# Kernel tuning notes

Measured on AMD Instinct MI355X. Metric: run time of the kernel, lower is better.

The kernel has to match this reference:

```python
import jax, jax.numpy as jnp
import numpy as np
import math

B, N, P, S, C, NC = 8, 20000, 256, 32, 256, 18


def setup_inputs() -> dict:
    key = jax.random.key(0)
    ks = jax.random.split(key, 20)
    w = lambda k, shape: jax.random.normal(k, shape, jnp.float32) * 0.02
    return {
        "xyz": jax.random.normal(ks[0], (B, N, 3), jnp.float32),
        "features": jax.random.normal(ks[1], (B, C, N), jnp.float32),
        "boxes_size": jax.random.uniform(ks[2], (B, P, 3), jnp.float32, 0.2, 1.5),
        "boxes_label": jax.random.normal(ks[3], (B, P, NC), jnp.float32),
        "ts": jax.random.uniform(ks[4], (B,), jnp.float32) * 1000.0,
        "inds": jax.random.randint(ks[5], (B, P), 0, N, jnp.int32),
        # SharedMLP (259 -> 128 -> 128 -> 128), bn=False so conv1x1+bias+ReLU
        "mw0": w(ks[6], (128, C + 3)), "mb0": jnp.zeros((128,), jnp.float32),
        "mw1": w(ks[7], (128, 128)), "mb1": jnp.zeros((128,), jnp.float32),
        "mw2": w(ks[8], (128, 128)), "mb2": jnp.zeros((128,), jnp.float32),
        # label SharedMLP (18+128 -> 256 -> 256 -> 256)
        "lw0": w(ks[9], (256, NC + 128)), "lb0": jnp.zeros((256,), jnp.float32),
        "lw1": w(ks[10], (256, 256)), "lb1": jnp.zeros((256,), jnp.float32),
        "lw2": w(ks[11], (256, 256)), "lb2": jnp.zeros((256,), jnp.float32),
        # time_mlp: sinusoid(128) -> 512 -> GELU -> 512 ; block: SiLU -> 256
        "tw0": w(ks[12], (512, 128)), "tb0": jnp.zeros((512,), jnp.float32),
        "tw1": w(ks[13], (512, 512)), "tb1": jnp.zeros((512,), jnp.float32),
        "bw": w(ks[14], (256, 512)), "bb": jnp.zeros((256,), jnp.float32),
        # time_mlp_label: sinusoid(256) -> 1024 -> GELU -> 1024 ; block: SiLU -> 512
        "tlw0": w(ks[15], (1024, 256)), "tlb0": jnp.zeros((1024,), jnp.float32),
        "tlw1": w(ks[16], (1024, 1024)), "tlb1": jnp.zeros((1024,), jnp.float32),
        "blw": w(ks[17], (512, 1024)), "blb": jnp.zeros((512,), jnp.float32),
    }


def _sinusoid(t, dim):
    half = dim // 2
    freqs = jnp.exp(jnp.arange(half, dtype=jnp.float32) * (-(math.log(10000.0) / (half - 1))))
    e = t[:, None] * freqs[None, :]
    return jnp.concatenate([jnp.sin(e), jnp.cos(e)], axis=-1)


def _film(feat, ts, w0, b0, w1, b1, bw, bb, dim):
    # feat: [B, D, P]; replicates torch repeat_interleave/chunk/reshape exactly
    temb = jax.nn.gelu(_sinusoid(ts, dim) @ w0.T + b0, approximate=False) @ w1.T + b1
    ss = jax.nn.silu(temb) @ bw.T + bb          # [B, 2D]
    ss = jnp.repeat(ss, P, axis=0)              # [B*P, 2D]
    scale, shift = jnp.split(ss, 2, axis=1)
    scale = scale.reshape(-1, P)
    shift = shift.reshape(-1, P)
    f = feat.reshape(-1, P)
    return (f * (scale + 1.0) + shift).reshape(feat.shape[0], -1, P)


def reference(xyz, features, boxes_size, boxes_label, ts, inds,
              mw0, mb0, mw1, mb1, mw2, mb2,
              lw0, lb0, lw1, lb1, lw2, lb2,
              tw0, tb0, tw1, tb1, bw, bb,
              tlw0, tlb0, tlw1, tlb1, blw, blb):
    # gather proposal centers
    new_xyz = jnp.take_along_axis(xyz, inds[:, :, None], axis=1)        # [B,P,3]
    # axis-aligned box containment (the hull corners are an AABB: center +/- size/2)
    half = boxes_size * 0.5
    inside = jnp.all(jnp.abs(xyz[:, None, :, :] - new_xyz[:, :, None, :]) <= half[:, :, None, :], axis=-1)  # [B,P,N]
    # deterministic with-replacement sampling of in-box points: in-box indices first (stable sort), then cycle
    order = jnp.argsort(jnp.logical_not(inside), axis=-1)               # [B,P,N]
    count = jnp.maximum(inside.sum(axis=-1), 1)                          # [B,P]
    pos = jnp.arange(S, dtype=count.dtype)[None, None, :] % count[:, :, None]
    idx = jnp.take_along_axis(order, pos, axis=-1)                       # [B,P,S]
    b_idx = jnp.arange(B)[:, None, None]
    gxyz = xyz[b_idx, idx] - new_xyz[:, :, None, :]                      # [B,P,S,3]
    gfeat = jnp.transpose(features, (0, 2, 1))[b_idx, idx]               # [B,P,S,C]
    g = jnp.concatenate([gxyz, gfeat], axis=-1)                          # [B,P,S,3+C]
    act = lambda x, w, b: jax.nn.relu(jnp.einsum('bpsc,oc->bpso', x, w) + b)
    h = act(act(act(g, mw0, mb0), mw1, mb1), mw2, mb2)                   # [B,P,S,128]
    nf = h.max(axis=2)                                                   # [B,P,128] (max-pool over nsample)
    nf_t = jnp.transpose(nf, (0, 2, 1))                                  # [B,128,P]
    new_features = _film(nf_t, ts, tw0, tb0, tw1, tb1, bw, bb, 128)
    # label branch
    li = jnp.concatenate([boxes_label, nf], axis=-1)                     # [B,P,18+128]
    act2 = lambda x, w, b: jax.nn.relu(jnp.einsum('bpc,oc->bpo', x, w) + b)
    lf = act2(act2(act2(li, lw0, lb0), lw1, lb1), lw2, lb2)              # [B,P,256]
    lf_t = jnp.transpose(lf, (0, 2, 1))                                  # [B,256,P]
    label_feature = _film(lf_t, ts, tlw0, tlb0, tlw1, tlb1, blw, blb, 256)
    return (new_xyz, new_features, label_feature, inds)
```

## Files before the change

kernel.cpp:

```cpp
#include <hip/hip_runtime.h>
#include <math.h>

#define BB 8
#define NN 20000
#define PP 256
#define SSAMP 32
#define CC 256

typedef unsigned short u16;
typedef unsigned int u32;
typedef __attribute__((ext_vector_type(8))) short short8;
typedef __attribute__((ext_vector_type(4))) float f32x4;

struct __align__(4) f3v { float x, y, z; };

__device__ __forceinline__ float b2f(u16 u) {
    union { u32 i; float f; } x; x.i = ((u32)u) << 16; return x.f;
}
__device__ __forceinline__ u16 f2b(float f) {
    union { float f; u32 i; } x; x.f = f;
    u32 i = x.i;
    i += 0x7fffu + ((i >> 16) & 1u);
    return (u16)(i >> 16);
}
__device__ __forceinline__ float rnd_bf(float f) { return b2f(f2b(f)); }
__device__ __forceinline__ float geluf(float x) {
    return 0.5f * x * (1.0f + erff(x * 0.7071067811865476f));
}
__device__ __forceinline__ float siluf(float x) {
    return x / (1.0f + expf(-x));
}
__device__ __forceinline__ f32x4 fz4() { f32x4 z = {0.f,0.f,0.f,0.f}; return z; }

__device__ __forceinline__ float ldf(const void* p, size_t i, int f32f) {
    return f32f ? ((const float*)p)[i] : b2f(((const u16*)p)[i]);
}
__device__ __forceinline__ u16 ldw(const void* p, size_t i, int f32f) {
    return f32f ? f2b(((const float*)p)[i]) : ((const u16*)p)[i];
}

__device__ __forceinline__ int detect_f32d(const void* xyz) {
    int lane = threadIdx.x & 63;
    u16 u = ((const u16*)xyz)[(size_t)lane * 7496];
    int e = (u >> 7) & 0xFF;
    bool inR = (e >= 0x70) && (e <= 0x85);
    unsigned long long m = __ballot(inR);
    return (__popcll(m) < 48) ? 1 : 0;
}

__device__ __forceinline__ void repack_body(int f32f, int rb, int tid,
        const void* mw0, const void* mw1, const void* mw2,
        const void* lw0, const void* lw1, const void* lw2,
        const void* mb0, const void* mb1, const void* mb2,
        const void* lb0, const void* lb1, const void* lb2,
        u16* __restrict__ W0p, u16* __restrict__ W1p, u16* __restrict__ W2p,
        u16* __restrict__ L0p, u16* __restrict__ L1p, u16* __restrict__ L2p,
        float* __restrict__ biasF) {
    int i = rb * 256 + tid;
    if (i < 36864) {
        int o = i / 288, c = i % 288;
        u16 v = 0;
        if (c < 256) v = ldw(mw0, o * 259 + 3 + c, f32f);
        else if (c < 259) v = ldw(mw0, o * 259 + (c - 256), f32f);
        W0p[i] = v;
    } else if (i < 53248) {
        W1p[i - 36864] = ldw(mw1, i - 36864, f32f);
    } else if (i < 69632) {
        W2p[i - 53248] = ldw(mw2, i - 53248, f32f);
    } else if (i < 110592) {
        int j = i - 69632;
        int o = j / 160, c = j % 160;
        L0p[j] = (c < 146) ? ldw(lw0, o * 146 + c, f32f) : (u16)0;
    } else if (i < 176128) {
        L1p[i - 110592] = ldw(lw1, i - 110592, f32f);
    } else if (i < 241664) {
        L2p[i - 176128] = ldw(lw2, i - 176128, f32f);
    } else if (i < 242816) {
        int j = i - 241664;
        float v;
        if (j < 128) v = ldf(mb0, j, f32f);
        else if (j < 256) v = ldf(mb1, j - 128, f32f);
        else if (j < 384) v = ldf(mb2, j - 256, f32f);
        else if (j < 640) v = ldf(lb0, j - 384, f32f);
        else if (j < 896) v = ldf(lb1, j - 640, f32f);
        else v = ldf(lb2, j - 896, f32f);
        biasF[j] = v;
    }
}

__device__ __forceinline__ void transpose_body(int f32f, const void* __restrict__ feat,
        u16* __restrict__ featT, int n0i, int c0i, int bz, int b0, int tid,
        u16 (*tile)[66]) {
    int c0 = c0i * 64, n0 = n0i * 64;
    int b = b0 + bz;
    const size_t fb = (size_t)b * CC * NN;
    const size_t tb = (size_t)bz * NN * CC;
    if (n0 + 64 <= NN) {
        int n4 = tid & 15, ci = tid >> 4;
        if (f32f) {
            #pragma unroll
            for (int pass = 0; pass < 4; pass++) {
                int c = pass * 16 + ci;
                const float* src = (const float*)feat + fb + (size_t)(c0 + c) * NN + n0 + n4 * 4;
                float4 v = *(const float4*)src;
                tile[c][n4 * 4 + 0] = f2b(v.x);
                tile[c][n4 * 4 + 1] = f2b(v.y);
                tile[c][n4 * 4 + 2] = f2b(v.z);
                tile[c][n4 * 4 + 3] = f2b(v.w);
            }
        } else {
            #pragma unroll
            for (int pass = 0; pass < 4; pass++) {
                int c = pass * 16 + ci;
                const u16* src = (const u16*)feat + fb + (size_t)(c0 + c) * NN + n0 + n4 * 4;
                ushort4 v = *(const ushort4*)src;
                tile[c][n4 * 4 + 0] = v.x;
                tile[c][n4 * 4 + 1] = v.y;
                tile[c][n4 * 4 + 2] = v.z;
                tile[c][n4 * 4 + 3] = v.w;
            }
        }
        __syncthreads();
        int c4 = tid & 15, ni = tid >> 4;
        #pragma unroll
        for (int pass = 0; pass < 4; pass++) {
            int n = pass * 16 + ni;
            ushort4 o;
            o.x = tile[c4 * 4 + 0][n];
            o.y = tile[c4 * 4 + 1][n];
            o.z = tile[c4 * 4 + 2][n];
            o.w = tile[c4 * 4 + 3][n];
            *(ushort4*)(featT + tb + (size_t)(n0 + n) * CC + c0 + c4 * 4) = o;
        }
    } else {
        int tx = tid & 63, ty = tid >> 6;
        for (int i = 0; i < 16; i++) {
            int cl = ty * 16 + i;
            int n = n0 + tx;
            if (n < NN) tile[cl][tx] = ldw(feat, fb + (size_t)(c0 + cl) * NN + n, f32f);
        }
        __syncthreads();
        for (int i = 0; i < 16; i++) {
            int nl = ty * 16 + i;
            int n = n0 + nl;
            if (n < NN) featT[tb + (size_t)n * CC + c0 + tx] = tile[tx][nl];
        }
    }
}

template<int ACT, int SRC>
__device__ __forceinline__ void lin_body(int f32f, const void* __restrict__ xin,
        const void* __restrict__ W, const void* __restrict__ bias,
        float* __restrict__ out, int K, int O, int rb, int tid, float* xs) {
    if (SRC == 2) {
        const float* X = (const float*)xin;
        for (int i = tid; i < 8 * K; i += 256) xs[i] = X[i];
    } else {
        const int half = (SRC == 0) ? 64 : 128;
        const int dim = half * 2;
        const float cst = (SRC == 0) ? (logf(10000.f) / 63.f) : (logf(10000.f) / 127.f);
        for (int i = tid; i < 8 * dim; i += 256) {
            int b = i / dim, j = i % dim;
            float t = ldf(xin, b, f32f);
            int jj = (j < half) ? j : (j - half);
            float e = t * expf(-(float)jj * cst);
            xs[i] = (j < half) ? sinf(e) : cosf(e);
        }
    }
    __syncthreads();
    int lane = tid & 63, wv = tid >> 6;
    int r = rb * 4 + wv;
    if (r >= O) return;
    float acc[8] = {0.f, 0.f, 0.f, 0.f, 0.f, 0.f, 0.f, 0.f};
    for (int k = lane; k < K; k += 64) {
        float wval = ldf(W, (size_t)r * K + k, f32f);
        #pragma unroll
        for (int b = 0; b < 8; b++) acc[b] += wval * xs[b * K + k];
    }
    #pragma unroll
    for (int b = 0; b < 8; b++) {
        acc[b] += __shfl_xor(acc[b], 1);
        acc[b] += __shfl_xor(acc[b], 2);
        acc[b] += __shfl_xor(acc[b], 4);
        acc[b] += __shfl_xor(acc[b], 8);
        acc[b] += __shfl_xor(acc[b], 16);
        acc[b] += __shfl_xor(acc[b], 32);
    }
    if (lane == 0) {
        float bv = ldf(bias, r, f32f);
        #pragma unroll
        for (int b = 0; b < 8; b++) {
            float v = acc[b] + bv;
            if (ACT == 1) v = geluf(v);
            else if (ACT == 2) v = siluf(v);
            out[b * O + r] = v;
        }
    }
}

__device__ __forceinline__ void sample_body(int f32f, const void* __restrict__ xyz,
        const void* __restrict__ bsize, const int* __restrict__ inds,
        int* __restrict__ sidx, float* __restrict__ cenW,
        float* __restrict__ outXyz, float* __restrict__ outInds,
        int pg, int tid, int* sBuf, int* wcnt) {
    int lane = tid & 63, w = tid >> 6;
    int b = pg >> 8;
    int ind = inds[pg];
    ind = ind < 0 ? 0 : (ind >= NN ? NN - 1 : ind);
    if (tid < SSAMP) sBuf[tid] = 0;
    size_t xb = (size_t)b * NN * 3;
    const f3v* Pts = (const f3v*)((const float*)xyz + xb);
    float cx, cy, cz;
    if (f32f) {
        f3v c = Pts[ind];
        cx = c.x; cy = c.y; cz = c.z;
    } else {
        cx = b2f(((const u16*)xyz)[xb + (size_t)ind * 3 + 0]);
        cy = b2f(((const u16*)xyz)[xb + (size_t)ind * 3 + 1]);
        cz = b2f(((const u16*)xyz)[xb + (size_t)ind * 3 + 2]);
    }
    float hx = 0.5f * ldf(bsize, pg * 3 + 0, f32f);
    float hy = 0.5f * ldf(bsize, pg * 3 + 1, f32f);
    float hz = 0.5f * ldf(bsize, pg * 3 + 2, f32f);
    int cnt = 0, par = 0;
    const unsigned long long lmask = (1ull << lane) - 1ull;
    for (int base = 0; base < NN; base += 1024, par ^= 4) {
        int nb = base + w * 256 + lane;
        int nn[4];
        float px[4], py[4], pz[4];
        #pragma unroll
        for (int u = 0; u < 4; u++) {
            int n = nb + u * 64;
            nn[u] = n;
            int nc = n < NN ? n : NN - 1;
            if (f32f) {
                f3v v = Pts[nc];
                px[u] = v.x; py[u] = v.y; pz[u] = v.z;
            } else {
                size_t a = xb + (size_t)nc * 3;
                px[u] = b2f(((const u16*)xyz)[a]);
                py[u] = b2f(((const u16*)xyz)[a + 1]);
                pz[u] = b2f(((const u16*)xyz)[a + 2]);
            }
        }
        bool isin[4];
        unsigned long long m[4];
        int pc[4];
        int tw = 0;
        #pragma unroll
        for (int u = 0; u < 4; u++) {
            bool in_ = (nn[u] < NN) &&
                       (fabsf(px[u] - cx) <= hx) &&
                       (fabsf(py[u] - cy) <= hy) &&
                       (fabsf(pz[u] - cz) <= hz);
            isin[u] = in_;
            m[u] = __ballot(in_);
            pc[u] = (int)__popcll(m[u]);
            tw += pc[u];
        }
        if (lane == 0) wcnt[par + w] = tw;
        __syncthreads();
        int w0 = wcnt[par + 0], w1 = wcnt[par + 1], w2 = wcnt[par + 2], w3 = wcnt[par + 3];
        int total = w0 + w1 + w2 + w3;
        int prior = cnt;
        if (w >= 1) prior += w0;
        if (w >= 2) prior += w1;
        if (w >= 3) prior += w2;
        #pragma unroll
        for (int u = 0; u < 4; u++) {
            int pos = prior + (int)__popcll(m[u] & lmask);
            if (isin[u] && pos < SSAMP) sBuf[pos] = nn[u];
            prior += pc[u];
        }
        cnt += total;
        if (cnt >= SSAMP) break;
    }
    __syncthreads();
    int ccap = cnt < SSAMP ? cnt : SSAMP;
    if (ccap < 1) ccap = 1;
    if (tid < SSAMP) sidx[pg * SSAMP + tid] = sBuf[tid % ccap];
    if (tid < 3) {
        float cv = tid == 0 ? cx : (tid == 1 ? cy : cz);
        outXyz[pg * 3 + tid] = cv;
        cenW[pg * 3 + tid] = cv;
    }
    if (tid == 0) outInds[pg] = rnd_bf((float)ind);
}

__device__ __forceinline__ void mlp1_body(int f32f,
        const u16* __restrict__ featT, const void* __restrict__ feat,
        int pbase, int tier,
        const void* __restrict__ xyz, const int* __restrict__ sidx,
        const float* __restrict__ cenW,
        const u16* __restrict__ W0p, const u16* __restrict__ W1p,
        const u16* __restrict__ W2p, const float* __restrict__ biasF,
        u16* __restrict__ nfB, float* __restrict__ nfF,
        int tid, u16* gA, int* nrowS, float* centS) {
    int b = pbase >> 8;
    if (tid < 64) {
        int n = sidx[pbase * SSAMP + tid];
        nrowS[tid] = n < 0 ? 0 : (n >= NN ? NN - 1 : n);
    }
    if (tid < 6) centS[tid] = cenW[pbase * 3 + tid];
    for (int e = tid; e < 64 * 32; e += 256) {
        int row = e >> 5, c2 = e & 31;
        if (c2 >= 8 && c2 < 28)
            *(u32*)&gA[row * 296 + 256 + (c2 - 8) * 2] = 0u;
    }
    __syncthreads();
    if (tier >= 1) {
        size_t rowBase = (tier == 2) ? ((size_t)b * NN) : 0;
        for (int e = tid; e < 64 * 32; e += 256) {
            int row = e >> 5, seg = e & 31;
            int n = nrowS[row];
            uint4 v = *(const uint4*)(featT + (rowBase + n) * CC + seg * 8);
            *(uint4*)&gA[row * 296 + seg * 8] = v;
        }
    } else {
        int row = tid & 63;
        int n = nrowS[row];
        const size_t fb = (size_t)b * CC * NN;
        int cbase = tid >> 6;
        for (int it = 0; it < 64; it++) {
            int cch = it * 4 + cbase;
            gA[row * 296 + cch] = ldw(feat, fb + (size_t)cch * NN + n, f32f);
        }
    }
    if (tid < 64) {
        int row = tid, q = row >> 5;
        int n = nrowS[row];
        size_t a = ((size_t)b * NN + n) * 3;
        for (int d = 0; d < 3; d++) {
            float gv = ldf(xyz, a + d, f32f) - centS[q * 3 + d];
            gA[row * 296 + 256 + d] = f2b(gv);
        }
    }
    __syncthreads();

    int lane = tid & 63, w = tid >> 6;
    int c15 = lane & 15, kq = lane >> 4;
    f32x4 acc[4][2];

    for (int mt = 0; mt < 4; mt++) for (int j = 0; j < 2; j++) acc[mt][j] = fz4();
    for (int ks = 0; ks < 9; ks++) {
        int k0 = ks * 32 + kq * 8;
        short8 af[4];
        for (int mt = 0; mt < 4; mt++)
            af[mt] = *(const short8*)&gA[(mt * 16 + c15) * 296 + k0];
        for (int j = 0; j < 2; j++) {
            int col = w * 32 + j * 16 + c15;
            short8 bf = *(const short8*)(W0p + col * 288 + k0);
            for (int mt = 0; mt < 4; mt++)
                acc[mt][j] = __builtin_amdgcn_mfma_f32_16x16x32_bf16(af[mt], bf, acc[mt][j], 0, 0, 0);
        }
    }
    __syncthreads();
    u16* h1s = gA;
    u16* h2s = gA + 8704;
    for (int j = 0; j < 2; j++) {
        int col = w * 32 + j * 16 + c15;
        float bias = biasF[col];
        for (int mt = 0; mt < 4; mt++)
            for (int r = 0; r < 4; r++) {
                float v = acc[mt][j][r] + bias;
                v = v > 0.f ? v : 0.f;
                h1s[(mt * 16 + kq * 4 + r) * 136 + col] = f2b(v);
            }
    }
    __syncthreads();

    for (int mt = 0; mt < 4; mt++) for (int j = 0; j < 2; j++) acc[mt][j] = fz4();
    for (int ks = 0; ks < 4; ks++) {
        int k0 = ks * 32 + kq * 8;
        short8 af[4];
        for (int mt = 0; mt < 4; mt++)
            af[mt] = *(const short8*)&h1s[(mt * 16 + c15) * 136 + k0];
        for (int j = 0; j < 2; j++) {
            int col = w * 32 + j * 16 + c15;
            short8 bf = *(const short8*)(W1p + col * 128 + k0);
            for (int mt = 0; mt < 4; mt++)
                acc[mt][j] = __builtin_amdgcn_mfma_f32_16x16x32_bf16(af[mt], bf, acc[mt][j], 0, 0, 0);
        }
    }
    __syncthreads();
    for (int j = 0; j < 2; j++) {
        int col = w * 32 + j * 16 + c15;
        float bias = biasF[128 + col];
        for (int mt = 0; mt < 4; mt++)
            for (int r = 0; r < 4; r++) {
                float v = acc[mt][j][r] + bias;
                v = v > 0.f ? v : 0.f;
                h2s[(mt * 16 + kq * 4 + r) * 136 + col] = f2b(v);
            }
    }
    __syncthreads();

    for (int mt = 0; mt < 4; mt++) for (int j = 0; j < 2; j++) acc[mt][j] = fz4();
    for (int ks = 0; ks < 4; ks++) {
        int k0 = ks * 32 + kq * 8;
        short8 af[4];
        for (int mt = 0; mt < 4; mt++)
            af[mt] = *(const short8*)&h2s[(mt * 16 + c15) * 136 + k0];
        for (int j = 0; j < 2; j++) {
            int col = w * 32 + j * 16 + c15;
            short8 bf = *(const short8*)(W2p + col * 128 + k0);
            for (int mt = 0; mt < 4; mt++)
                acc[mt][j] = __builtin_amdgcn_mfma_f32_16x16x32_bf16(af[mt], bf, acc[mt][j], 0, 0, 0);
        }
    }
    int pA = pbase & 255, pB = (pbase + 1) & 255;
    for (int j = 0; j < 2; j++) {
        int col = w * 32 + j * 16 + c15;
        float bias = biasF[256 + col];
        float mA = 0.f, mB = 0.f;
        for (int mt = 0; mt < 2; mt++)
            for (int r = 0; r < 4; r++) {
                float v = acc[mt][j][r] + bias; v = v > 0.f ? v : 0.f;
                mA = fmaxf(mA, v);
            }
        for (int mt = 2; mt < 4; mt++)
            for (int r = 0; r < 4; r++) {
                float v = acc[mt][j][r] + bias; v = v > 0.f ? v : 0.f;
                mB = fmaxf(mB, v);
            }
        mA = fmaxf(mA, __shfl_xor(mA, 16)); mA = fmaxf(mA, __shfl_xor(mA, 32));
        mB = fmaxf(mB, __shfl_xor(mB, 16)); mB = fmaxf(mB, __shfl_xor(mB, 32));
        if (lane < 16) {
            nfB[(size_t)(pbase + 0) * 128 + col] = f2b(mA);
            nfB[(size_t)(pbase + 1) * 128 + col] = f2b(mB);
            nfF[((size_t)b * 128 + col) * 256 + pA] = mA;
            nfF[((size_t)b * 128 + col) * 256 + pB] = mB;
        }
    }
}

__global__ __launch_bounds__(256) void k_front(
        const void* __restrict__ xyz, const void* __restrict__ feat,
        const void* __restrict__ bsize, const int* __restrict__ inds,
        const void* __restrict__ ts,
        const void* mw0, const void* mw1, const void* mw2,
        const void* lw0, const void* lw1, const void* lw2,
        const void* mb0, const void* mb1, const void* mb2,
        const void* lb0, const void* lb1, const void* lb2,
        const void* tw0, const void* tb0,
        const void* tlw0, const void* tlb0,
        u16* __restrict__ featT, int nTrans,
        int* __restrict__ sidx, float* __restrict__ cenW,
        float* __restrict__ outXyz, float* __restrict__ outInds,
        u16* __restrict__ W0p, u16* __restrict__ W1p, u16* __restrict__ W2p,
        u16* __restrict__ L0p, u16* __restrict__ L1p, u16* __restrict__ L2p,
        float* __restrict__ biasF, float* __restrict__ h0W, float* __restrict__ g0W) {
    __shared__ __align__(16) char smem[8448];
    int tid = threadIdx.x;
    int f32f = detect_f32d(xyz);
    unsigned bx = blockIdx.x;
    if (nTrans > 0) {
        const unsigned NI = 7u * 2048u;
        if (bx < NI) {
            if (bx % 7u == 0u) {
                sample_body(f32f, xyz, bsize, inds, sidx, cenW, outXyz, outInds,
                            (int)(bx / 7u), tid, (int*)smem, (int*)(smem + 128));
            } else {
                int t = (int)(bx - bx / 7u - 1u);
                if (t < nTrans)
                    transpose_body(f32f, feat, featT, t % 313, (t / 313) & 3, t / 1252,
                                   0, tid, (u16(*)[66])smem);
            }
        } else if (bx < NI + 949u) {
            repack_body(f32f, (int)(bx - NI), tid, mw0, mw1, mw2, lw0, lw1, lw2,
                        mb0, mb1, mb2, lb0, lb1, lb2, W0p, W1p, W2p, L0p, L1p, L2p, biasF);
        } else if (bx < NI + 1077u) {
            lin_body<1, 0>(f32f, ts, tw0, tb0, h0W, 128, 512, (int)(bx - NI - 949u), tid, (float*)smem);
        } else {
            lin_body<1, 1>(f32f, ts, tlw0, tlb0, g0W, 256, 1024, (int)(bx - NI - 1077u), tid, (float*)smem);
        }
    } else {
        if (bx < 2048u) {
            sample_body(f32f, xyz, bsize, inds, sidx, cenW, outXyz, outInds,
                        (int)bx, tid, (int*)smem, (int*)(smem + 128));
        } else if (bx < 2997u) {
            repack_body(f32f, (int)(bx - 2048u), tid, mw0, mw1, mw2, lw0, lw1, lw2,
                        mb0, mb1, mb2, lb0, lb1, lb2, W0p, W1p, W2p, L0p, L1p, L2p, biasF);
        } else if (bx < 3125u) {
            lin_body<1, 0>(f32f, ts, tw0, tb0, h0W, 128, 512, (int)(bx - 2997u), tid, (float*)smem);
        } else {
            lin_body<1, 1>(f32f, ts, tlw0, tlb0, g0W, 256, 1024, (int)(bx - 3125u), tid, (float*)smem);
        }
    }
}

__global__ __launch_bounds__(256) void k_mid(int nMlp, int blockOff, int tier,
        const u16* __restrict__ featT, const void* __restrict__ feat,
        const void* __restrict__ xyz, const int* __restrict__ sidx,
        const float* __restrict__ cenW,
        const u16* __restrict__ W0p, const u16* __restrict__ W1p,
        const u16* __restrict__ W2p, const float* __restrict__ biasF,
        u16* __restrict__ nfB, float* __restrict__ nfF,
        const void* tw1, const void* tb1, const void* tlw1, const void* tlb1,
        const float* __restrict__ h0W, const float* __restrict__ g0W,
        float* __restrict__ tembW, float* __restrict__ temblW) {
    __shared__ __align__(16) char smem[38176];
    int tid = threadIdx.x;
    int f32f = detect_f32d(xyz);
    int bx = (int)blockIdx.x;
    if (bx < nMlp) {
        mlp1_body(f32f, featT, feat, (bx + blockOff) * 2, tier, xyz, sidx, cenW,
                  W0p, W1p, W2p, biasF, nfB, nfF, tid,
                  (u16*)smem, (int*)(smem + 37888), (float*)(smem + 38144));
    } else {
        int lb = bx - nMlp;
        float* xs = (float*)smem;
        if (lb < 128) lin_body<2, 2>(f32f, h0W, tw1, tb1, tembW, 512, 512, lb, tid, xs);
        else lin_body<2, 2>(f32f, g0W, tlw1, tlb1, temblW, 1024, 1024, lb - 128, tid, xs);
    }
}

__global__ __launch_bounds__(256) void k_lin3(const void* __restrict__ xyz,
        const void* bw, const void* bb, const void* blw, const void* blb,
        const float* __restrict__ tembW, const float* __restrict__ temblW,
        float* __restrict__ ssW, float* __restrict__ sslW) {
    __shared__ float xs[8 * 1024];
    int tid = threadIdx.x;
    int f32f = detect_f32d(xyz);
    unsigned bx = blockIdx.x;
    if (bx < 64u) lin_body<0, 2>(f32f, tembW, bw, bb, ssW, 512, 256, (int)bx, tid, xs);
    else lin_body<0, 2>(f32f, temblW, blw, blb, sslW, 1024, 512, (int)(bx - 64u), tid, xs);
}

__global__ __launch_bounds__(256) void k_transpose(const void* __restrict__ xyz,
                                                   const void* __restrict__ feat,
                                                   u16* __restrict__ featT, int b0) {
    __shared__ u16 tile[64][66];
    int f32f = detect_f32d(xyz);
    transpose_body(f32f, feat, featT, blockIdx.x, blockIdx.y, blockIdx.z, b0,
                   threadIdx.x, tile);
}

__global__ __launch_bounds__(256) void k_tail(const void* __restrict__ xyz,
        const void* __restrict__ blabel,
        const u16* __restrict__ nfB, const u16* __restrict__ L0p,
        const u16* __restrict__ L1p, const u16* __restrict__ L2p,
        const float* __restrict__ biasF, const float* __restrict__ sslW,
        const float* __restrict__ ssW, const float* __restrict__ nfF,
        float* __restrict__ outLF, float* __restrict__ outNF) {
    __shared__ u16 liS[16 * 168];
    __shared__ u16 h1L[16 * 264];
    __shared__ u16 h2L[16 * 264];
    int f32f = detect_f32d(xyz);
    int tid = threadIdx.x;
    unsigned bxu = blockIdx.x;
    if (bxu >= 128u) {
        int base = (int)(bxu - 128u) * 4096;
        #pragma unroll
        for (int i = 0; i < 16; i++) {
            int idx = base + i * 256 + tid;
            int p = idx & 255;
            int cb = idx >> 8;
            int b = cb >> 7;
            float sc = ssW[b * 256 + (p & 127)] + 1.f;
            float sh = ssW[b * 256 + 128 + (p & 127)];
            outNF[idx] = nfF[idx] * sc + sh;
        }
        return;
    }
    int pbase = (int)bxu * 16;
    for (int e = tid; e < 16 * 160; e += 256) {
        int row = e / 160, c = e % 160;
        int pg = pbase + row;
        u16 v = 0;
        if (c < 18) v = ldw(blabel, pg * 18 + c, f32f);
        else if (c < 146) v = nfB[(size_t)pg * 128 + (c - 18)];
        liS[row * 168 + c] = v;
    }
    __syncthreads();
    int lane = tid & 63, w = tid >> 6;
    int c15 = lane & 15, kq = lane >> 4;
    f32x4 acc[4];

    for (int j = 0; j < 4; j++) acc[j] = fz4();
    for (int ks = 0; ks < 5; ks++) {
        int k0 = ks * 32 + kq * 8;
        short8 af = *(const short8*)&liS[c15 * 168 + k0];
        for (int j = 0; j < 4; j++) {
            int col = w * 64 + j * 16 + c15;
            short8 bf = *(const short8*)(L0p + col * 160 + k0);
            acc[j] = __builtin_amdgcn_mfma_f32_16x16x32_bf16(af, bf, acc[j], 0, 0, 0);
        }
    }
    for (int j = 0; j < 4; j++) {
        int col = w * 64 + j * 16 + c15;
        float bias = biasF[384 + col];
        for (int r = 0; r < 4; r++) {
            float v = acc[j][r] + bias; v = v > 0.f ? v : 0.f;
            h1L[(kq * 4 + r) * 264 + col] = f2b(v);
        }
    }
    __syncthreads();

    for (int j = 0; j < 4; j++) acc[j] = fz4();
    for (int ks = 0; ks < 8; ks++) {
        int k0 = ks * 32 + kq * 8;
        short8 af = *(const short8*)&h1L[c15 * 264 + k0];
        for (int j = 0; j < 4; j++) {
            int col = w * 64 + j * 16 + c15;
            short8 bf = *(const short8*)(L1p + col * 256 + k0);
            acc[j] = __builtin_amdgcn_mfma_f32_16x16x32_bf16(af, bf, acc[j], 0, 0, 0);
        }
    }
    for (int j = 0; j < 4; j++) {
        int col = w * 64 + j * 16 + c15;
        float bias = biasF[640 + col];
        for (int r = 0; r < 4; r++) {
            float v = acc[j][r] + bias; v = v > 0.f ? v : 0.f;
            h2L[(kq * 4 + r) * 264 + col] = f2b(v);
        }
    }
    __syncthreads();

    for (int j = 0; j < 4; j++) acc[j] = fz4();
    for (int ks = 0; ks < 8; ks++) {
        int k0 = ks * 32 + kq * 8;
        short8 af = *(const short8*)&h2L[c15 * 264 + k0];
        for (int j = 0; j < 4; j++) {
            int col = w * 64 + j * 16 + c15;
            short8 bf = *(const short8*)(L2p + col * 256 + k0);
            acc[j] = __builtin_amdgcn_mfma_f32_16x16x32_bf16(af, bf, acc[j], 0, 0, 0);
        }
    }
    for (int j = 0; j < 4; j++) {
        int col = w * 64 + j * 16 + c15;
        float bias = biasF[896 + col];
        for (int r = 0; r < 4; r++) {
            int pr = pbase + kq * 4 + r;
            int bb2 = pr >> 8, p = pr & 255;
            float v = acc[j][r] + bias; v = v > 0.f ? v : 0.f;
            float sc = sslW[bb2 * 512 + p] + 1.f;
            float sh = sslW[bb2 * 512 + 256 + p];
            outLF[((size_t)bb2 * 256 + col) * 256 + p] = v * sc + sh;
        }
    }
}

extern "C" void kernel_launch(void* const* d_in, const int* in_sizes, int n_in,
                              void* d_out, int out_size, void* d_ws, size_t ws_size,
                              hipStream_t stream) {
    const void* xyz    = d_in[0];
    const void* feat   = d_in[1];
    const void* bsize  = d_in[2];
    const void* blabel = d_in[3];
    const void* ts     = d_in[4];
    const int* inds    = (const int*)d_in[5];
    const void* mw0 = d_in[6];  const void* mb0 = d_in[7];
    const void* mw1 = d_in[8];  const void* mb1 = d_in[9];
    const void* mw2 = d_in[10]; const void* mb2 = d_in[11];
    const void* lw0 = d_in[12]; const void* lb0 = d_in[13];
    const void* lw1 = d_in[14]; const void* lb1 = d_in[15];
    const void* lw2 = d_in[16]; const void* lb2 = d_in[17];
    const void* tw0 = d_in[18]; const void* tb0 = d_in[19];
    const void* tw1 = d_in[20]; const void* tb1 = d_in[21];
    const void* bw  = d_in[22]; const void* bb  = d_in[23];
    const void* tlw0 = d_in[24]; const void* tlb0 = d_in[25];
    const void* tlw1 = d_in[26]; const void* tlb1 = d_in[27];
    const void* blw  = d_in[28]; const void* blb  = d_in[29];

    float* out = (float*)d_out;
    float* outXyz  = out;
    float* outNF   = out + 6144;
    float* outLF   = out + 268288;
    float* outInds = out + 792576;

    char* ws = (char*)d_ws;
    u16*   W0p   = (u16*)(ws + 64);
    u16*   W1p   = (u16*)(ws + 73792);
    u16*   W2p   = (u16*)(ws + 106560);
    u16*   L0p   = (u16*)(ws + 139328);
    u16*   L1p   = (u16*)(ws + 221248);
    u16*   L2p   = (u16*)(ws + 352320);
    float* biasF = (float*)(ws + 483392);
    float* ssW   = (float*)(ws + 488000);
    float* sslW  = (float*)(ws + 496192);
    float* cenW  = (float*)(ws + 512576);
    int*   sidx  = (int*)(ws + 537152);
    u16*   nfB   = (u16*)(ws + 799296);
    float* h0W   = (float*)(ws + 1323584);
    float* tembW = (float*)(ws + 1339968);
    float* g0W   = (float*)(ws + 1356352);
    float* temblW= (float*)(ws + 1389120);
    float* nfF   = (float*)(ws + 1421888);
    u16*   featT = (u16*)(ws + 2470464);
    const size_t NEED_A = 2470464ull + 81920000ull;
    const size_t NEED_B = 2470464ull + 10240000ull;
    int tier = (ws_size >= NEED_A) ? 2 : ((ws_size >= NEED_B) ? 1 : 0);

    int nTrans = (tier == 2) ? 10016 : 0;
    unsigned gFront = (nTrans > 0) ? (7u * 2048u + 949u + 384u)
                                   : (2048u + 949u + 384u);
    k_front<<<dim3(gFront), dim3(256), 0, stream>>>(
        xyz, feat, bsize, inds, ts,
        mw0, mw1, mw2, lw0, lw1, lw2,
        mb0, mb1, mb2, lb0, lb1, lb2,
        tw0, tb0, tlw0, tlb0,
        featT, nTrans, sidx, cenW, outXyz, outInds,
        W0p, W1p, W2p, L0p, L1p, L2p, biasF, h0W, g0W);

    if (tier == 2) {
        k_mid<<<dim3(1024 + 384), dim3(256), 0, stream>>>(1024, 0, 2,
            featT, feat, xyz, sidx, cenW, W0p, W1p, W2p, biasF, nfB, nfF,
            tw1, tb1, tlw1, tlb1, h0W, g0W, tembW, temblW);
    } else if (tier == 1) {
        for (int b = 0; b < BB; b++) {
            k_transpose<<<dim3(313, 4, 1), dim3(256), 0, stream>>>(xyz, feat, featT, b);
            k_mid<<<dim3(128), dim3(256), 0, stream>>>(128, b * 128, 1,
                featT, feat, xyz, sidx, cenW, W0p, W1p, W2p, biasF, nfB, nfF,
                tw1, tb1, tlw1, tlb1, h0W, g0W, tembW, temblW);
        }
        k_mid<<<dim3(384), dim3(256), 0, stream>>>(0, 0, 1,
            featT, feat, xyz, sidx, cenW, W0p, W1p, W2p, biasF, nfB, nfF,
            tw1, tb1, tlw1, tlb1, h0W, g0W, tembW, temblW);
    } else {
        k_mid<<<dim3(1024 + 384), dim3(256), 0, stream>>>(1024, 0, 0,
            featT, feat, xyz, sidx, cenW, W0p, W1p, W2p, biasF, nfB, nfF,
            tw1, tb1, tlw1, tlb1, h0W, g0W, tembW, temblW);
    }

    k_lin3<<<dim3(192), dim3(256), 0, stream>>>(xyz, bw, bb, blw, blb,
                                                tembW, temblW, ssW, sslW);

    k_tail<<<dim3(128 + 64), dim3(256), 0, stream>>>(xyz, blabel, nfB,
        L0p, L1p, L2p, biasF, sslW, ssW, nfF, outLF, outNF);
}
```

Baseline: 417.7 us.

## Fuse FiLM scale/shift linear into tail kernel and widen ball-query sampling stride

Removes the separate k_lin3 launch. Each k_tail block now computes only the FiLM scale/shift rows it needs, from SiLU of the time embedding, directly into shared memory. This saves one kernel launch and a global round trip, but some work is repeated: every outNF block recomputes all 256 rows of a 512-wide matvec. The box sampling loop also scans 4096 points per iteration with 16 points per thread, which halves-to-quarters the barrier count but uses more registers and overshoots on early exit.

```diff
diff --git a/kernel.cpp b/kernel.cpp
--- a/kernel.cpp
+++ b/kernel.cpp
@@ -202,7 +202,7 @@
         const void* __restrict__ bsize, const int* __restrict__ inds,
         int* __restrict__ sidx, float* __restrict__ cenW,
         float* __restrict__ outXyz, float* __restrict__ outInds,
-        int pg, int tid, int* sBuf, int* wcnt) {
+        int pg, int tid, int* sBuf, int* wcnt ) {
     int lane = tid & 63, w = tid >> 6;
     int b = pg >> 8;
     int ind = inds[pg];
@@ -224,55 +224,55 @@
     float hz = 0.5f * ldf(bsize, pg * 3 + 2, f32f);
     int cnt = 0, par = 0;
     const unsigned long long lmask = (1ull << lane) - 1ull;
-    for (int base = 0; base < NN; base += 1024, par ^= 4) {
-        int nb = base + w * 256 + lane;
-        int nn[4];
-        float px[4], py[4], pz[4];
+    for (int base = 0; base < NN; base += 4096, par ^= 64) {
+        u32 inmask = 0;
+        {
+            float px[16], py[16], pz[16];
+            #pragma unroll
+            for (int u = 0; u < 16; u++) {
+                int n = base + u * 256 + tid;
+                int nc = n < NN ? n : NN - 1;
+                if (f32f) {
+                    f3v v = Pts[nc];
+                    px[u] = v.x; py[u] = v.y; pz[u] = v.z;
+                } else {
+                    size_t a = xb + (size_t)nc * 3;
+                    px[u] = b2f(((const u16*)xyz)[a]);
+                    py[u] = b2f(((const u16*)xyz)[a + 1]);
+                    pz[u] = b2f(((const u16*)xyz)[a + 2]);
+                }
+            }
+            #pragma unroll
+            for (int u = 0; u < 16; u++) {
+                bool in_ = (base + u * 256 + tid < NN) &&
+                           (fabsf(px[u] - cx) <= hx) &&
+                           (fabsf(py[u] - cy) <= hy) &&
+                           (fabsf(pz[u] - cz) <= hz);
+                inmask |= ((u32)in_) << u;
+            }
+        }
         #pragma unroll
-        for (int u = 0; u < 4; u++) {
-            int n = nb + u * 64;
-            nn[u] = n;
-            int nc = n < NN ? n : NN - 1;
-            if (f32f) {
-                f3v v = Pts[nc];
-                px[u] = v.x; py[u] = v.y; pz[u] = v.z;
-            } else {
-                size_t a = xb + (size_t)nc * 3;
-                px[u] = b2f(((const u16*)xyz)[a]);
-                py[u] = b2f(((const u16*)xyz)[a + 1]);
-                pz[u] = b2f(((const u16*)xyz)[a + 2]);
-            }
-        }
-        bool isin[4];
-        unsigned long long m[4];
-        int pc[4];
-        int tw = 0;
+        for (int u = 0; u < 16; u++) {
+            unsigned long long m = __ballot((inmask >> u) & 1u);
+            if (lane == 0) wcnt[par + w * 16 + u] = (int)__popcll(m);
+        }
+        __syncthreads();
+        int run = cnt;
         #pragma unroll
-        for (int u = 0; u < 4; u++) {
-            bool in_ = (nn[u] < NN) &&
-                       (fabsf(px[u] - cx) <= hx) &&
-                       (fabsf(py[u] - cy) <= hy) &&
-                       (fabsf(pz[u] - cz) <= hz);
-            isin[u] = in_;
-            m[u] = __ballot(in_);
-            pc[u] = (int)__popcll(m[u]);
-            tw += pc[u];
-        }
-        if (lane == 0) wcnt[par + w] = tw;
-        __syncthreads();
-        int w0 = wcnt[par + 0], w1 = wcnt[par + 1], w2 = wcnt[par + 2], w3 = wcnt[par + 3];
-        int total = w0 + w1 + w2 + w3;
-        int prior = cnt;
-        if (w >= 1) prior += w0;
-        if (w >= 2) prior += w1;
-        if (w >= 3) prior += w2;
-        #pragma unroll
-        for (int u = 0; u < 4; u++) {
-            int pos = prior + (int)__popcll(m[u] & lmask);
-            if (isin[u] && pos < SSAMP) sBuf[pos] = nn[u];
-            prior += pc[u];
-        }
-        cnt += total;
+        for (int u = 0; u < 16; u++) {
+            int c0 = wcnt[par + u];
+            int c1 = wcnt[par + 16 + u];
+            int c2 = wcnt[par + 32 + u];
+            int c3 = wcnt[par + 48 + u];
+            unsigned long long m = __ballot((inmask >> u) & 1u);
+            if ((inmask >> u) & 1u) {
+                int priorw = (w > 0 ? c0 : 0) + (w > 1 ? c1 : 0) + (w > 2 ? c2 : 0);
+                int pos = run + priorw + (int)__popcll(m & lmask);
+                if (pos < SSAMP) sBuf[pos] = base + u * 256 + tid;
+            }
+            run += c0 + c1 + c2 + c3;
+        }
+        cnt = run;
         if (cnt >= SSAMP) break;
     }
     __syncthreads();
@@ -515,18 +515,6 @@
     }
 }
 
-__global__ __launch_bounds__(256) void k_lin3(const void* __restrict__ xyz,
-        const void* bw, const void* bb, const void* blw, const void* blb,
-        const float* __restrict__ tembW, const float* __restrict__ temblW,
-        float* __restrict__ ssW, float* __restrict__ sslW) {
-    __shared__ float xs[8 * 1024];
-    int tid = threadIdx.x;
-    int f32f = detect_f32d(xyz);
-    unsigned bx = blockIdx.x;
-    if (bx < 64u) lin_body<0, 2>(f32f, tembW, bw, bb, ssW, 512, 256, (int)bx, tid, xs);
-    else lin_body<0, 2>(f32f, temblW, blw, blb, sslW, 1024, 512, (int)(bx - 64u), tid, xs);
-}
-
 __global__ __launch_bounds__(256) void k_transpose(const void* __restrict__ xyz,
                                                    const void* __restrict__ feat,
                                                    u16* __restrict__ featT, int b0) {
@@ -540,30 +528,56 @@
         const void* __restrict__ blabel,
         const u16* __restrict__ nfB, const u16* __restrict__ L0p,
         const u16* __restrict__ L1p, const u16* __restrict__ L2p,
-        const float* __restrict__ biasF, const float* __restrict__ sslW,
-        const float* __restrict__ ssW, const float* __restrict__ nfF,
+        const float* __restrict__ biasF,
+        const void* bw, const void* bb, const void* blw, const void* blb,
+        const float* __restrict__ tembW, const float* __restrict__ temblW,
+        const float* __restrict__ nfF,
         float* __restrict__ outLF, float* __restrict__ outNF) {
-    __shared__ u16 liS[16 * 168];
-    __shared__ u16 h1L[16 * 264];
-    __shared__ u16 h2L[16 * 264];
+    __shared__ __align__(16) char smemT[26496];
     int f32f = detect_f32d(xyz);
     int tid = threadIdx.x;
+    int lane = tid & 63, w = tid >> 6;
     unsigned bxu = blockIdx.x;
     if (bxu >= 128u) {
-        int base = (int)(bxu - 128u) * 4096;
+        float* sl2 = (float*)smemT;
+        float* swS = (float*)smemT + 512;
+        int t = (int)(bxu - 128u);
+        int base = t * 4096;
+        int b = (base >> 8) >> 7;
+        for (int i = tid; i < 512; i += 256) sl2[i] = siluf(tembW[b * 512 + i]);
+        __syncthreads();
+        for (int i = 0; i < 64; i++) {
+            int r = w * 64 + i;
+            float a = 0.f;
+            for (int k = lane; k < 512; k += 64)
+                a += ldf(bw, (size_t)r * 512 + k, f32f) * sl2[k];
+            a += __shfl_xor(a, 1);
+            a += __shfl_xor(a, 2);
+            a += __shfl_xor(a, 4);
+            a += __shfl_xor(a, 8);
+            a += __shfl_xor(a, 16);
+            a += __shfl_xor(a, 32);
+            if (lane == 0) swS[r] = a + ldf(bb, r, f32f);
+        }
+        __syncthreads();
         #pragma unroll
         for (int i = 0; i < 16; i++) {
             int idx = base + i * 256 + tid;
             int p = idx & 255;
-            int cb = idx >> 8;
-            int b = cb >> 7;
-            float sc = ssW[b * 256 + (p & 127)] + 1.f;
-            float sh = ssW[b * 256 + 128 + (p & 127)];
+            float sc = swS[p & 127] + 1.f;
+            float sh = swS[128 + (p & 127)];
             outNF[idx] = nfF[idx] * sc + sh;
         }
         return;
     }
+    u16* liS = (u16*)smemT;
+    u16* h1L = (u16*)(smemT + 5376);
+    u16* h2L = (u16*)(smemT + 13824);
+    float* slS = (float*)(smemT + 22272);
+    float* sslS = (float*)(smemT + 26368);
     int pbase = (int)bxu * 16;
+    int bb2 = pbase >> 8;
+    int p0 = pbase & 255;
     for (int e = tid; e < 16 * 160; e += 256) {
         int row = e / 160, c = e % 160;
         int pg = pbase + row;
@@ -572,8 +586,22 @@
         else if (c < 146) v = nfB[(size_t)pg * 128 + (c - 18)];
         liS[row * 168 + c] = v;
     }
-    __syncthreads();
-    int lane = tid & 63, w = tid >> 6;
+    for (int i = tid; i < 1024; i += 256) slS[i] = siluf(temblW[bb2 * 1024 + i]);
+    __syncthreads();
+    for (int i = 0; i < 8; i++) {
+        int j = w * 8 + i;
+        int r = (j < 16) ? (p0 + j) : (256 + p0 + (j - 16));
+        float a = 0.f;
+        for (int k = lane; k < 1024; k += 64)
+            a += ldf(blw, (size_t)r * 1024 + k, f32f) * slS[k];
+        a += __shfl_xor(a, 1);
+        a += __shfl_xor(a, 2);
+        a += __shfl_xor(a, 4);
+        a += __shfl_xor(a, 8);
+        a += __shfl_xor(a, 16);
+        a += __shfl_xor(a, 32);
+        if (lane == 0) sslS[j] = a + ldf(blb, r, f32f);
+    }
     int c15 = lane & 15, kq = lane >> 4;
     f32x4 acc[4];
 
@@ -631,11 +659,12 @@
         int col = w * 64 + j * 16 + c15;
         float bias = biasF[896 + col];
         for (int r = 0; r < 4; r++) {
-            int pr = pbase + kq * 4 + r;
-            int bb2 = pr >> 8, p = pr & 255;
+            int jj = kq * 4 + r;
+            int pr = pbase + jj;
+            int p = pr & 255;
             float v = acc[j][r] + bias; v = v > 0.f ? v : 0.f;
-            float sc = sslW[bb2 * 512 + p] + 1.f;
-            float sh = sslW[bb2 * 512 + 256 + p];
+            float sc = sslS[jj] + 1.f;
+            float sh = sslS[16 + jj];
             outLF[((size_t)bb2 * 256 + col) * 256 + p] = v * sc + sh;
         }
     }
@@ -677,8 +706,6 @@
     u16*   L1p   = (u16*)(ws + 221248);
     u16*   L2p   = (u16*)(ws + 352320);
     float* biasF = (float*)(ws + 483392);
-    float* ssW   = (float*)(ws + 488000);
-    float* sslW  = (float*)(ws + 496192);
     float* cenW  = (float*)(ws + 512576);
     int*   sidx  = (int*)(ws + 537152);
     u16*   nfB   = (u16*)(ws + 799296);
@@ -723,9 +750,7 @@
             tw1, tb1, tlw1, tlb1, h0W, g0W, tembW, temblW);
     }
 
-    k_lin3<<<dim3(192), dim3(256), 0, stream>>>(xyz, bw, bb, blw, blb,
-                                                tembW, temblW, ssW, sslW);
-
     k_tail<<<dim3(128 + 64), dim3(256), 0, stream>>>(xyz, blabel, nfB,
-        L0p, L1p, L2p, biasF, sslW, ssW, nfF, outLF, outNF);
-}
+        L0p, L1p, L2p, biasF, bw, bb, blw, blb, tembW, temblW, nfF,
+        outLF, outNF);
+}
```

Result: slower. 603.5 us (+44.5%).
